# Kernel tuning notes

Hardware: AMD Instinct MI355X
Metric: run time of the kernel (lower is better)

The kernel has to match this reference:

```python
import jax, jax.numpy as jnp
import numpy as np

B, S, D = 4, 4096, 256

def setup_inputs() -> dict:
    key = jax.random.key(0)
    kx, kq, kk, kv = jax.random.split(key, 4)
    # torch nn.Linear(D, D) weight init: U(-1/sqrt(D), 1/sqrt(D)), stored as [out, in]
    bound = 1.0 / np.sqrt(D)
    x = jax.random.normal(kx, (B, S, D), dtype=jnp.float32)
    Wq = jax.random.uniform(kq, (D, D), dtype=jnp.float32, minval=-bound, maxval=bound)
    Wk = jax.random.uniform(kk, (D, D), dtype=jnp.float32, minval=-bound, maxval=bound)
    Wv = jax.random.uniform(kv, (D, D), dtype=jnp.float32, minval=-bound, maxval=bound)
    return {"x": x, "Wq": Wq, "Wk": Wk, "Wv": Wv}

def reference(x, Wq, Wk, Wv):
    # Linear with weight [out,in]: y = x @ W^T
    Q = jnp.einsum('bsd,ed->bse', x, Wq)
    K = jnp.einsum('bsd,ed->bse', x, Wk)
    V = jnp.einsum('bsd,ed->bse', x, Wv)
    d = x.shape[-1]
    scores = jnp.einsum('bqe,bke->bqk', Q, K) / jnp.sqrt(jnp.float32(d))  # [B,S,S]
    S_len = x.shape[1]
    causal = jnp.tril(jnp.ones((S_len, S_len), dtype=bool))
    scores = jnp.where(causal, scores, -jnp.inf)
    attn = jax.nn.softmax(scores, axis=-1)
    return jnp.einsum('bqk,bke->bqe', attn, V)
```

## Files before the change

### kernel.cpp

```cpp
#include <hip/hip_runtime.h>

typedef unsigned short u16;
typedef unsigned int u32;
typedef __attribute__((ext_vector_type(8))) short bf16x8;
typedef __attribute__((ext_vector_type(4))) float f32x4;
typedef __attribute__((ext_vector_type(16))) float f32x16;

#define MFMA16 __builtin_amdgcn_mfma_f32_16x16x32_bf16
#define MFMA32 __builtin_amdgcn_mfma_f32_32x32x16_bf16

__device__ __forceinline__ u16 f2bf(float f) {
  u32 u = __builtin_bit_cast(u32, f);
  u = u + 0x7FFFu + ((u >> 16) & 1u);
  return (u16)(u >> 16);
}
__device__ __forceinline__ u32 pk2(float lo, float hi) {
  return (u32)f2bf(lo) | ((u32)f2bf(hi) << 16);
}
__device__ __forceinline__ float bf2f(u32 x) {
  return __builtin_bit_cast(float, x << 16);
}
__device__ __forceinline__ u32 cvtpk(float lo, float hi) {
  u32 r;
  asm("v_cvt_pk_bf16_f32 %0, %1, %2" : "=v"(r) : "v"(lo), "v"(hi));
  return r;
}
__device__ __forceinline__ void pswap(u32& x, u32& y) {
  asm("v_permlane32_swap_b32 %0, %1" : "+v"(x), "+v"(y));
}
__device__ __forceinline__ void gld16(const void* gp, void* lp) {
  __builtin_amdgcn_global_load_lds((const __attribute__((address_space(1))) u32*)gp,
                                   (__attribute__((address_space(3))) u32*)lp, 16, 0, 0);
}

__global__ __launch_bounds__(256) void cvt_kernel(
    const float* __restrict__ x, const float* __restrict__ wq,
    const float* __restrict__ wk, const float* __restrict__ wv,
    u16* __restrict__ xbf, u16* __restrict__ wbf) {
  int idx = blockIdx.x * 256 + threadIdx.x;
  if (idx < 1048576) {
    float4 v = ((const float4*)x)[idx];
    uint2 u; u.x = pk2(v.x, v.y); u.y = pk2(v.z, v.w);
    ((uint2*)xbf)[idx] = u;
  } else {
    int j = idx - 1048576;
    const float* W = (j < 16384) ? wq : (j < 32768) ? wk : wv;
    int k = j & 16383;
    float4 v = ((const float4*)W)[k];
    uint2 u; u.x = pk2(v.x, v.y); u.y = pk2(v.z, v.w);
    ((uint2*)wbf)[j] = u;
  }
}

__global__ __launch_bounds__(256, 2) void proj_kernel(
    const u16* __restrict__ xbf, const u16* __restrict__ wbf,
    u16* __restrict__ Qs, u16* __restrict__ Ks, u16* __restrict__ Vt) {
  int tile = blockIdx.x, mat = blockIdx.y;
  int tid = threadIdx.x, w = tid >> 6, lane = tid & 63, b15 = lane & 15, g = lane >> 4;
  int base = tile * 64 + w * 16;
  const u16* W = wbf + mat * 65536;
  const u16* Xp = xbf + (size_t)(base + b15) * 256;
  f32x4 acc[16] = {};
  if (mat < 2) {
#pragma unroll
    for (int kk = 0; kk < 8; ++kk) {
      bf16x8 xf = *(const bf16x8*)(Xp + kk * 32 + g * 8);
#pragma unroll
      for (int eb = 0; eb < 16; ++eb) {
        bf16x8 wf = *(const bf16x8*)(W + (size_t)(eb * 16 + b15) * 256 + kk * 32 + g * 8);
        acc[eb] = MFMA16(xf, wf, acc[eb], 0, 0, 0);
      }
    }
    float scale = (mat == 0) ? 0.0901684400555602f : 1.0f;
    u16* dst = (mat == 0) ? Qs : Ks;
#pragma unroll
    for (int eb = 0; eb < 16; ++eb)
#pragma unroll
      for (int r = 0; r < 4; ++r)
        dst[(size_t)(base + g * 4 + r) * 256 + eb * 16 + b15] = f2bf(acc[eb][r] * scale);
  } else {
#pragma unroll
    for (int kk = 0; kk < 8; ++kk) {
      bf16x8 xf = *(const bf16x8*)(Xp + kk * 32 + g * 8);
#pragma unroll
      for (int eb = 0; eb < 16; ++eb) {
        bf16x8 wf = *(const bf16x8*)(W + (size_t)(eb * 16 + b15) * 256 + kk * 32 + g * 8);
        acc[eb] = MFMA16(wf, xf, acc[eb], 0, 0, 0);
      }
    }
    int sglob = base + b15;
    int b = sglob >> 12, sl = sglob & 4095;
#pragma unroll
    for (int eb = 0; eb < 16; ++eb)
#pragma unroll
      for (int r = 0; r < 4; ++r) {
        int e = eb * 16 + g * 4 + r;
        Vt[((size_t)(b * 256 + e) << 12) + sl] = f2bf(acc[eb][r]);
      }
  }
}

__global__ __launch_bounds__(256, 2) void attn_kernel(
    const u16* __restrict__ Qs, const u16* __restrict__ Ks_,
    const u16* __restrict__ Vt_, u16* __restrict__ pacc, float2* __restrict__ pml) {
  __shared__ u16 Kd[2][8192];
  __shared__ u16 Vd[2][8192];

  int bid = blockIdx.x;
  int xcd = bid & 7;
  int b = xcd >> 1;
  int u = (bid >> 3) * 2 + (xcd & 1);
  int g4 = 0;
#pragma unroll
  for (int t = 1; t <= 7; ++t) g4 += (u >= 2 * t * (t + 1)) ? 1 : 0;
  int v = u - 2 * g4 * (g4 + 1);
  int tt = 4 * g4 + v / (g4 + 1);
  int c = v % (g4 + 1);
  int uid = b * 144 + u;

  int tid = threadIdx.x, w = tid >> 6, lane = tid & 63;
  int l31 = lane & 31, h = lane >> 5;
  int qbase = tt * 128 + w * 32;
  int qrow = qbase + l31;
  int kt0 = c * 16, kt_end = min(kt0 + 16, 4 * (tt + 1));

  int Koff[4], Voff[4];
#pragma unroll
  for (int i = 0; i < 4; ++i) {
    int o = (w * 4 + i) * 1024 + lane * 16;
    int row = o >> 9;
    Koff[i] = row * 512 + ((o & 511) ^ ((row & 15) << 4));
    int e = o >> 6;
    Voff[i] = e * 8192 + ((o & 63) ^ ((e & 3) << 4));
  }
  const char* Kgb = (const char*)(Ks_ + (size_t)b * 4096 * 256);
  const char* Vgb = (const char*)(Vt_ + (size_t)b * 1048576);
  char* KL = (char*)&Kd[0][0];
  char* VL = (char*)&Vd[0][0];

  auto stage = [&](int buf, int kt) {
    size_t kb = (size_t)kt * 32 * 512;
    size_t vb = (size_t)kt * 64;
#pragma unroll
    for (int i = 0; i < 4; ++i)
      gld16(Kgb + kb + Koff[i], KL + buf * 16384 + (w * 4 + i) * 1024);
#pragma unroll
    for (int i = 0; i < 4; ++i)
      gld16(Vgb + vb + Voff[i], VL + buf * 16384 + (w * 4 + i) * 1024);
  };

  const u16* Qrow = Qs + ((size_t)b * 4096 + qrow) * 256;
  bf16x8 qf[16];
#pragma unroll
  for (int kc = 0; kc < 16; ++kc)
    qf[kc] = *(const bf16x8*)(Qrow + kc * 16 + h * 8);

  f32x16 acc[8] = {};
  float m0 = -3e38f, l0 = 0.f;
  stage(0, kt0);
  int cur = 0;

  for (int kt = kt0; kt < kt_end; ++kt) {
    __syncthreads();
    if (kt + 1 < kt_end) stage(cur ^ 1, kt + 1);
    int kv0 = kt * 32;
    if (kv0 <= qbase + 31) {
      const char* Kc = KL + cur * 16384;
      const char* Vc = VL + cur * 16384;
      f32x16 sA = {}, sB = {};
      __builtin_amdgcn_s_setprio(1);
#pragma unroll
      for (int kc = 0; kc < 16; kc += 2) {
        bf16x8 k0 = *(const bf16x8*)(Kc + l31 * 512 + ((kc * 32 + h * 16) ^ ((l31 & 15) << 4)));
        bf16x8 k1 = *(const bf16x8*)(Kc + l31 * 512 + (((kc + 1) * 32 + h * 16) ^ ((l31 & 15) << 4)));
        sA = MFMA32(k0, qf[kc], sA, 0, 0, 0);
        sB = MFMA32(k1, qf[kc + 1], sB, 0, 0, 0);
      }
      __builtin_amdgcn_s_setprio(0);
      f32x16 s = sA + sB;
      if (kv0 + 31 > qbase) {
#pragma unroll
        for (int r = 0; r < 16; ++r) {
          int kv = kv0 + (r & 3) + 8 * (r >> 2) + 4 * h;
          if (kv > qrow) s[r] = -3e38f;
        }
      }
      float pm = s[0];
#pragma unroll
      for (int r = 1; r < 16; ++r) pm = fmaxf(pm, s[r]);
      pm = fmaxf(pm, __shfl_xor(pm, 32));
      if (__any(pm > m0 + 8.f)) {
        float mn = fmaxf(m0, pm);
        float sc = exp2f(m0 - mn);
        l0 *= sc;
#pragma unroll
        for (int et = 0; et < 8; ++et) acc[et] *= sc;
        m0 = mn;
      }
      float p[16];
#pragma unroll
      for (int r = 0; r < 16; ++r) {
        p[r] = exp2f(s[r] - m0);
        l0 += p[r];
      }
      u32 w0 = cvtpk(p[0], p[1]),  w1 = cvtpk(p[2], p[3]);
      u32 w2 = cvtpk(p[4], p[5]),  w3 = cvtpk(p[6], p[7]);
      u32 w4 = cvtpk(p[8], p[9]),  w5 = cvtpk(p[10], p[11]);
      u32 w6 = cvtpk(p[12], p[13]), w7 = cvtpk(p[14], p[15]);
      pswap(w0, w2); pswap(w1, w3);
      pswap(w4, w6); pswap(w5, w7);
      union { u32 uu[4]; bf16x8 vv; } pA, pB;
      pA.uu[0] = w0; pA.uu[1] = w1; pA.uu[2] = w2; pA.uu[3] = w3;
      pB.uu[0] = w4; pB.uu[1] = w5; pB.uu[2] = w6; pB.uu[3] = w7;
      __builtin_amdgcn_s_setprio(1);
#pragma unroll
      for (int et = 0; et < 8; ++et) {
        const char* vrow = Vc + (et * 32 + l31) * 64;
        bf16x8 vf0 = *(const bf16x8*)(vrow + ((h * 16) ^ ((l31 & 3) << 4)));
        bf16x8 vf1 = *(const bf16x8*)(vrow + ((32 + h * 16) ^ ((l31 & 3) << 4)));
        acc[et] = MFMA32(vf0, pA.vv, acc[et], 0, 0, 0);
        acc[et] = MFMA32(vf1, pB.vv, acc[et], 0, 0, 0);
      }
      __builtin_amdgcn_s_setprio(0);
    }
    cur ^= 1;
  }

  l0 += __shfl_xor(l0, 32);

  u16* ppr = pacc + ((size_t)uid * 128 + w * 32 + l31) * 256;
#pragma unroll
  for (int et = 0; et < 8; ++et)
#pragma unroll
    for (int j = 0; j < 4; ++j) {
      uint2 o;
      o.x = pk2(acc[et][4 * j], acc[et][4 * j + 1]);
      o.y = pk2(acc[et][4 * j + 2], acc[et][4 * j + 3]);
      *(uint2*)(ppr + et * 32 + 8 * j + 4 * h) = o;
    }
  if (h == 0) {
    float2 a; a.x = m0; a.y = l0;
    pml[(size_t)uid * 128 + w * 32 + l31] = a;
  }
}

__global__ __launch_bounds__(256) void combine_kernel(
    const u16* __restrict__ pacc, const float2* __restrict__ pml,
    float* __restrict__ out) {
  int row = blockIdx.x * 4 + (threadIdx.x >> 6);
  int lane = threadIdx.x & 63;
  int b = row >> 12, r = row & 4095;
  int tt = r >> 7, rin = r & 127;
  int g4 = tt >> 2, nch = g4 + 1;
  int ubase = b * 144 + 2 * g4 * (g4 + 1) + (tt & 3) * (g4 + 1);
  float M = -3e38f;
  for (int cc = 0; cc < nch; ++cc)
    M = fmaxf(M, pml[(size_t)(ubase + cc) * 128 + rin].x);
  float L = 0.f, o0 = 0.f, o1 = 0.f, o2 = 0.f, o3 = 0.f;
  for (int cc = 0; cc < nch; ++cc) {
    float2 ml = pml[(size_t)(ubase + cc) * 128 + rin];
    float s = exp2f(ml.x - M);
    L += ml.y * s;
    uint2 a = *(const uint2*)(pacc + ((size_t)(ubase + cc) * 128 + rin) * 256 + lane * 4);
    o0 += s * bf2f(a.x & 0xffffu); o1 += s * bf2f(a.x >> 16);
    o2 += s * bf2f(a.y & 0xffffu); o3 += s * bf2f(a.y >> 16);
  }
  float inv = 1.f / L;
  f32x4 res = {o0 * inv, o1 * inv, o2 * inv, o3 * inv};
  *(f32x4*)(out + (size_t)row * 256 + lane * 4) = res;
}

extern "C" void kernel_launch(void* const* d_in, const int* in_sizes, int n_in,
                              void* d_out, int out_size, void* d_ws, size_t ws_size,
                              hipStream_t stream) {
  const float* x = (const float*)d_in[0];
  const float* wq = (const float*)d_in[1];
  const float* wk = (const float*)d_in[2];
  const float* wv = (const float*)d_in[3];
  char* ws = (char*)d_ws;
  u16* xbf = (u16*)(ws);
  u16* wbf = (u16*)(ws + 8388608);
  u16* Qs  = (u16*)(ws + 9437184);
  u16* Ks  = (u16*)(ws + 17825792);
  u16* Vt  = (u16*)(ws + 26214400);
  u16* pacc = (u16*)(ws + 34603008);
  float2* pml = (float2*)(ws + 72351744);
  float* out = (float*)d_out;

  hipLaunchKernelGGL(cvt_kernel, dim3(4288), dim3(256), 0, stream, x, wq, wk, wv, xbf, wbf);
  hipLaunchKernelGGL(proj_kernel, dim3(256, 3), dim3(256), 0, stream, xbf, wbf, Qs, Ks, Vt);
  hipLaunchKernelGGL(attn_kernel, dim3(576), dim3(256), 0, stream, Qs, Ks, Vt, pacc, pml);
  hipLaunchKernelGGL(combine_kernel, dim3(4096), dim3(256), 0, stream, pacc, pml, out);
}
```

Before: 178.6 us.

## Pair short causal attention work units into single blocks and retune V swizzle

Reworks the attention grid mapping so the shortest causal work units (the partial chunks with fewer key tiles) are paired two per block, shrinking the grid from 576 to 512 blocks. The goal is better load balance across CUs, with each block doing closer to a full chunk of work. The per-unit attention body moves into a lambda that is called once or twice. The V shared-memory swizzle also changes from (e&3) to ((e>>1)&3) to reduce LDS bank conflicts on the V reads. Paired blocks run two units back to back, which may lengthen the critical path if the pairing is uneven.

```diff
diff --git a/kernel.cpp b/kernel.cpp
--- a/kernel.cpp
+++ b/kernel.cpp
@@ -109,20 +109,24 @@
   int bid = blockIdx.x;
   int xcd = bid & 7;
   int b = xcd >> 1;
-  int u = (bid >> 3) * 2 + (xcd & 1);
-  int g4 = 0;
-#pragma unroll
-  for (int t = 1; t <= 7; ++t) g4 += (u >= 2 * t * (t + 1)) ? 1 : 0;
-  int v = u - 2 * g4 * (g4 + 1);
-  int tt = 4 * g4 + v / (g4 + 1);
-  int c = v % (g4 + 1);
-  int uid = b * 144 + u;
+  int j = ((bid >> 3) << 1) | (bid & 1);
+  int t0, c0, t1 = -1, c1 = 0;
+  if (j < 16) {
+    int g = j & 7;
+    if (j < 8) { t0 = 4 * g;     t1 = 4 * g + 3; }
+    else       { t0 = 4 * g + 1; t1 = 4 * g + 2; }
+    c0 = g; c1 = g;
+  } else {
+    int jj = j - 16;
+    int g = 1;
+#pragma unroll
+    for (int gg = 2; gg <= 7; ++gg) if (jj >= 2 * gg * (gg - 1)) g = gg;
+    int r = jj - 2 * g * (g - 1);
+    t0 = 4 * g + r / g; c0 = r % g;
+  }
 
   int tid = threadIdx.x, w = tid >> 6, lane = tid & 63;
   int l31 = lane & 31, h = lane >> 5;
-  int qbase = tt * 128 + w * 32;
-  int qrow = qbase + l31;
-  int kt0 = c * 16, kt_end = min(kt0 + 16, 4 * (tt + 1));
 
   int Koff[4], Voff[4];
 #pragma unroll
@@ -131,7 +135,7 @@
     int row = o >> 9;
     Koff[i] = row * 512 + ((o & 511) ^ ((row & 15) << 4));
     int e = o >> 6;
-    Voff[i] = e * 8192 + ((o & 63) ^ ((e & 3) << 4));
+    Voff[i] = e * 8192 + ((o & 63) ^ (((e >> 1) & 3) << 4));
   }
   const char* Kgb = (const char*)(Ks_ + (size_t)b * 4096 * 256);
   const char* Vgb = (const char*)(Vt_ + (size_t)b * 1048576);
@@ -149,98 +153,113 @@
       gld16(Vgb + vb + Voff[i], VL + buf * 16384 + (w * 4 + i) * 1024);
   };
 
-  const u16* Qrow = Qs + ((size_t)b * 4096 + qrow) * 256;
-  bf16x8 qf[16];
-#pragma unroll
-  for (int kc = 0; kc < 16; ++kc)
-    qf[kc] = *(const bf16x8*)(Qrow + kc * 16 + h * 8);
-
-  f32x16 acc[8] = {};
-  float m0 = -3e38f, l0 = 0.f;
-  stage(0, kt0);
-  int cur = 0;
-
-  for (int kt = kt0; kt < kt_end; ++kt) {
+  auto process = [&](int tt, int c) {
+    int g4 = tt >> 2;
+    int uid = b * 144 + 2 * g4 * (g4 + 1) + (tt & 3) * (g4 + 1) + c;
+    int qbase = tt * 128 + w * 32;
+    int qrow = qbase + l31;
+    int kt0 = 16 * c, kt_end = min(16 * c + 16, 4 * (tt + 1));
+
+    const u16* Qrow = Qs + ((size_t)b * 4096 + qrow) * 256;
+    bf16x8 qf[16];
+#pragma unroll
+    for (int kc = 0; kc < 16; ++kc)
+      qf[kc] = *(const bf16x8*)(Qrow + kc * 16 + h * 8);
+
+    f32x16 acc[8] = {};
+    float m0 = -3e38f, l0 = 0.f;
+    stage(0, kt0);
+    int cur = 0;
+
+    for (int kt = kt0; kt < kt_end; ++kt) {
+      __syncthreads();
+      if (kt + 1 < kt_end) stage(cur ^ 1, kt + 1);
+      int kv0 = kt * 32;
+      if (kv0 <= qbase + 31) {
+        const char* Kc = KL + cur * 16384;
+        const char* Vc = VL + cur * 16384;
+        f32x16 sA = {}, sB = {};
+        __builtin_amdgcn_s_setprio(1);
+#pragma unroll
+        for (int kc = 0; kc < 16; kc += 2) {
+          bf16x8 k0 = *(const bf16x8*)(Kc + l31 * 512 + ((kc * 32 + h * 16) ^ ((l31 & 15) << 4)));
+          bf16x8 k1 = *(const bf16x8*)(Kc + l31 * 512 + (((kc + 1) * 32 + h * 16) ^ ((l31 & 15) << 4)));
+          sA = MFMA32(k0, qf[kc], sA, 0, 0, 0);
+          sB = MFMA32(k1, qf[kc + 1], sB, 0, 0, 0);
+        }
+        __builtin_amdgcn_s_setprio(0);
+        f32x16 s = sA + sB;
+        if (kv0 + 31 > qbase) {
+#pragma unroll
+          for (int r = 0; r < 16; ++r) {
+            int kv = kv0 + (r & 3) + 8 * (r >> 2) + 4 * h;
+            if (kv > qrow) s[r] = -3e38f;
+          }
+        }
+        float pm = s[0];
+#pragma unroll
+        for (int r = 1; r < 16; ++r) pm = fmaxf(pm, s[r]);
+        pm = fmaxf(pm, __shfl_xor(pm, 32));
+        if (__any(pm > m0 + 8.f)) {
+          float mn = fmaxf(m0, pm);
+          float sc = exp2f(m0 - mn);
+          l0 *= sc;
+#pragma unroll
+          for (int et = 0; et < 8; ++et) acc[et] *= sc;
+          m0 = mn;
+        }
+        float p[16];
+#pragma unroll
+        for (int r = 0; r < 16; ++r) {
+          p[r] = exp2f(s[r] - m0);
+          l0 += p[r];
+        }
+        u32 w0 = cvtpk(p[0], p[1]),   w1 = cvtpk(p[2], p[3]);
+        u32 w2 = cvtpk(p[4], p[5]),   w3 = cvtpk(p[6], p[7]);
+        u32 w4 = cvtpk(p[8], p[9]),   w5 = cvtpk(p[10], p[11]);
+        u32 w6 = cvtpk(p[12], p[13]), w7 = cvtpk(p[14], p[15]);
+        pswap(w0, w2); pswap(w1, w3);
+        pswap(w4, w6); pswap(w5, w7);
+        union { u32 uu[4]; bf16x8 vv; } pA, pB;
+        pA.uu[0] = w0; pA.uu[1] = w1; pA.uu[2] = w2; pA.uu[3] = w3;
+        pB.uu[0] = w4; pB.uu[1] = w5; pB.uu[2] = w6; pB.uu[3] = w7;
+        __builtin_amdgcn_s_setprio(1);
+#pragma unroll
+        for (int et = 0; et < 8; ++et) {
+          const char* vrow = Vc + (et * 32 + l31) * 64;
+          int swz = ((l31 >> 1) & 3) << 4;
+          bf16x8 vf0 = *(const bf16x8*)(vrow + ((h * 16) ^ swz));
+          bf16x8 vf1 = *(const bf16x8*)(vrow + ((32 + h * 16) ^ swz));
+          acc[et] = MFMA32(vf0, pA.vv, acc[et], 0, 0, 0);
+          acc[et] = MFMA32(vf1, pB.vv, acc[et], 0, 0, 0);
+        }
+        __builtin_amdgcn_s_setprio(0);
+      }
+      cur ^= 1;
+    }
+
+    l0 += __shfl_xor(l0, 32);
+
+    u16* ppr = pacc + ((size_t)uid * 128 + w * 32 + l31) * 256;
+#pragma unroll
+    for (int et = 0; et < 8; ++et)
+#pragma unroll
+      for (int jj = 0; jj < 4; ++jj) {
+        uint2 o;
+        o.x = pk2(acc[et][4 * jj], acc[et][4 * jj + 1]);
+        o.y = pk2(acc[et][4 * jj + 2], acc[et][4 * jj + 3]);
+        *(uint2*)(ppr + et * 32 + 8 * jj + 4 * h) = o;
+      }
+    if (h == 0) {
+      float2 a; a.x = m0; a.y = l0;
+      pml[(size_t)uid * 128 + w * 32 + l31] = a;
+    }
+  };
+
+  process(t0, c0);
+  if (t1 >= 0) {
     __syncthreads();
-    if (kt + 1 < kt_end) stage(cur ^ 1, kt + 1);
-    int kv0 = kt * 32;
-    if (kv0 <= qbase + 31) {
-      const char* Kc = KL + cur * 16384;
-      const char* Vc = VL + cur * 16384;
-      f32x16 sA = {}, sB = {};
-      __builtin_amdgcn_s_setprio(1);
-#pragma unroll
-      for (int kc = 0; kc < 16; kc += 2) {
-        bf16x8 k0 = *(const bf16x8*)(Kc + l31 * 512 + ((kc * 32 + h * 16) ^ ((l31 & 15) << 4)));
-        bf16x8 k1 = *(const bf16x8*)(Kc + l31 * 512 + (((kc + 1) * 32 + h * 16) ^ ((l31 & 15) << 4)));
-        sA = MFMA32(k0, qf[kc], sA, 0, 0, 0);
-        sB = MFMA32(k1, qf[kc + 1], sB, 0, 0, 0);
-      }
-      __builtin_amdgcn_s_setprio(0);
-      f32x16 s = sA + sB;
-      if (kv0 + 31 > qbase) {
-#pragma unroll
-        for (int r = 0; r < 16; ++r) {
-          int kv = kv0 + (r & 3) + 8 * (r >> 2) + 4 * h;
-          if (kv > qrow) s[r] = -3e38f;
-        }
-      }
-      float pm = s[0];
-#pragma unroll
-      for (int r = 1; r < 16; ++r) pm = fmaxf(pm, s[r]);
-      pm = fmaxf(pm, __shfl_xor(pm, 32));
-      if (__any(pm > m0 + 8.f)) {
-        float mn = fmaxf(m0, pm);
-        float sc = exp2f(m0 - mn);
-        l0 *= sc;
-#pragma unroll
-        for (int et = 0; et < 8; ++et) acc[et] *= sc;
-        m0 = mn;
-      }
-      float p[16];
-#pragma unroll
-      for (int r = 0; r < 16; ++r) {
-        p[r] = exp2f(s[r] - m0);
-        l0 += p[r];
-      }
-      u32 w0 = cvtpk(p[0], p[1]),  w1 = cvtpk(p[2], p[3]);
-      u32 w2 = cvtpk(p[4], p[5]),  w3 = cvtpk(p[6], p[7]);
-      u32 w4 = cvtpk(p[8], p[9]),  w5 = cvtpk(p[10], p[11]);
-      u32 w6 = cvtpk(p[12], p[13]), w7 = cvtpk(p[14], p[15]);
-      pswap(w0, w2); pswap(w1, w3);
-      pswap(w4, w6); pswap(w5, w7);
-      union { u32 uu[4]; bf16x8 vv; } pA, pB;
-      pA.uu[0] = w0; pA.uu[1] = w1; pA.uu[2] = w2; pA.uu[3] = w3;
-      pB.uu[0] = w4; pB.uu[1] = w5; pB.uu[2] = w6; pB.uu[3] = w7;
-      __builtin_amdgcn_s_setprio(1);
-#pragma unroll
-      for (int et = 0; et < 8; ++et) {
-        const char* vrow = Vc + (et * 32 + l31) * 64;
-        bf16x8 vf0 = *(const bf16x8*)(vrow + ((h * 16) ^ ((l31 & 3) << 4)));
-        bf16x8 vf1 = *(const bf16x8*)(vrow + ((32 + h * 16) ^ ((l31 & 3) << 4)));
-        acc[et] = MFMA32(vf0, pA.vv, acc[et], 0, 0, 0);
-        acc[et] = MFMA32(vf1, pB.vv, acc[et], 0, 0, 0);
-      }
-      __builtin_amdgcn_s_setprio(0);
-    }
-    cur ^= 1;
-  }
-
-  l0 += __shfl_xor(l0, 32);
-
-  u16* ppr = pacc + ((size_t)uid * 128 + w * 32 + l31) * 256;
-#pragma unroll
-  for (int et = 0; et < 8; ++et)
-#pragma unroll
-    for (int j = 0; j < 4; ++j) {
-      uint2 o;
-      o.x = pk2(acc[et][4 * j], acc[et][4 * j + 1]);
-      o.y = pk2(acc[et][4 * j + 2], acc[et][4 * j + 3]);
-      *(uint2*)(ppr + et * 32 + 8 * j + 4 * h) = o;
-    }
-  if (h == 0) {
-    float2 a; a.x = m0; a.y = l0;
-    pml[(size_t)uid * 128 + w * 32 + l31] = a;
+    process(t1, c1);
   }
 }
 
@@ -289,6 +308,6 @@
 
   hipLaunchKernelGGL(cvt_kernel, dim3(4288), dim3(256), 0, stream, x, wq, wk, wv, xbf, wbf);
   hipLaunchKernelGGL(proj_kernel, dim3(256, 3), dim3(256), 0, stream, xbf, wbf, Qs, Ks, Vt);
-  hipLaunchKernelGGL(attn_kernel, dim3(576), dim3(256), 0, stream, Qs, Ks, Vt, pacc, pml);
+  hipLaunchKernelGGL(attn_kernel, dim3(512), dim3(256), 0, stream, Qs, Ks, Vt, pacc, pml);
   hipLaunchKernelGGL(combine_kernel, dim3(4096), dim3(256), 0, stream, pacc, pml, out);
 }
```

Result: faster. 157.1 us (-12.0%).
